# Performance work log

Measured on AMD Instinct MI355X. Metric: run time of the kernel, lower is better.

Reference implementation:

```python
import jax, jax.numpy as jnp
import numpy as np

N = 2048
T = 4000
MAX_SPIKES = 512
V_RESET = 1.0
ALPHA = 0.01


def setup_inputs() -> dict:
    key = jax.random.key(0)
    k1, k2, k3, k4, k5 = jax.random.split(key, 5)
    ts = jnp.arange(T, dtype=jnp.float32) * (1.0 / T)  # [T] grid over [0, 1)
    v0 = 0.1 * jax.random.normal(k1, (N,), dtype=jnp.float32)
    i0 = 0.1 * jax.random.normal(k2, (N,), dtype=jnp.float32)
    ic = jax.random.uniform(k3, (N,), dtype=jnp.float32, minval=0.5, maxval=1.5)
    # _build_w: uniform weights in [0.5, 1), network mask all-False -> no zeroing
    w = jax.random.uniform(k4, (N, N), dtype=jnp.float32, minval=0.5, maxval=1.0)
    mu = jax.random.uniform(k5, (2,), dtype=jnp.float32, minval=0.5, maxval=1.0)
    return {"ts": ts, "v0": v0, "i0": i0, "ic": ic, "w": w, "mu": mu,
            "seed": 0, "max_spikes": MAX_SPIKES}


def reference(ts, v0, i0, ic, w, mu, seed, max_spikes):
    n = v0.shape[0]
    key = jax.random.key(seed)
    k_init, k_trans = jax.random.split(key)
    # s0 = log(U) - alpha  (negative; spike when s crosses 0)
    s0 = jnp.log(jax.random.uniform(k_init, (n,))) - ALPHA
    y0 = jnp.stack([v0, i0, s0], axis=-1)  # [n, 3]

    dts = ts[1:] - ts[:-1]
    steps = jnp.arange(ts.shape[0] - 1)
    tev0 = jnp.full((max_spikes,), jnp.inf, dtype=ts.dtype)
    yev0 = jnp.full((max_spikes, n, 3), jnp.inf, dtype=y0.dtype)
    et0 = jnp.zeros((max_spikes, n), dtype=bool)

    def drift(y):
        v, i, s = y[:, 0], y[:, 1], y[:, 2]
        dv = mu[0] * (i + ic - v)
        di = -mu[1] * i
        ds = jax.nn.softplus(v)  # intensity_fn
        return jnp.stack([dv, di, ds], axis=-1)

    def step(carry, inp):
        y, nsp, tev, yev, et = carry
        t_next, dt, idx = inp
        y1 = y + dt * drift(y)                 # Euler step
        ev = y1[:, 2] >= 0.0                   # cond_fn: y[n, 2] root crossing
        has = jnp.any(ev)
        eidx = jnp.argmax(ev)
        u = jax.random.uniform(jax.random.fold_in(k_trans, idx), (n,))
        # trans_fn: reset v, add weight row to all i, resample s for spikers
        v_t = y1[:, 0] - jnp.where(ev, V_RESET, 0.0)
        i_t = y1[:, 1] + w[eidx]
        s_t = jnp.where(ev, jnp.log(u) - ALPHA, y1[:, 2])
        y2 = jnp.where(has, jnp.stack([v_t, i_t, s_t], axis=-1), y1)
        rec = has & (nsp < max_spikes)
        widx = jnp.minimum(nsp, max_spikes - 1)
        tev = tev.at[widx].set(jnp.where(rec, t_next, tev[widx]))
        yev = yev.at[widx].set(jnp.where(rec, y1, yev[widx]))
        et = et.at[widx].set(jnp.where(rec, ev, et[widx]))
        nsp = nsp + has.astype(jnp.int32)
        return (y2, nsp, tev, yev, et), y2

    init = (y0, jnp.int32(0), tev0, yev0, et0)
    (_, num_spikes, tevents, yevents, event_types), ys_rest = jax.lax.scan(
        step, init, (ts[1:], dts, steps))
    ys = jnp.concatenate([y0[None], ys_rest], axis=0)  # [T, n, 3]
    return ys, tevents, yevents, event_types, num_spikes
```

## Files before the change

### kernel.cpp

```cpp
#include <hip/hip_runtime.h>
#include <stdint.h>

#define XLA_LOG_TAIL_A 1
#define XLA_USE_FMA    0

#if XLA_USE_FMA
#define MADD(a,b,c) __builtin_fmaf((a),(b),(c))
#else
#define MADD(a,b,c) ((a)*(b)+(c))
#endif

#define N_NEUR 2048
#define HALF_N 1024
#define CKPT   125

__device__ __forceinline__ uint32_t rotl32(uint32_t x, int r) {
  return (x << r) | (x >> (32 - r));
}

__device__ __forceinline__ void tf2x32(uint32_t k0, uint32_t k1,
                                       uint32_t& x0, uint32_t& x1) {
  const uint32_t k2 = k0 ^ k1 ^ 0x1BD11BDAu;
  x0 += k0; x1 += k1;
#define TF_R(r) { x0 += x1; x1 = rotl32(x1, r); x1 ^= x0; }
  TF_R(13) TF_R(15) TF_R(26) TF_R(6)
  x0 += k1; x1 += k2 + 1u;
  TF_R(17) TF_R(29) TF_R(16) TF_R(24)
  x0 += k2; x1 += k0 + 2u;
  TF_R(13) TF_R(15) TF_R(26) TF_R(6)
  x0 += k0; x1 += k1 + 3u;
  TF_R(17) TF_R(29) TF_R(16) TF_R(24)
  x0 += k1; x1 += k2 + 4u;
  TF_R(13) TF_R(15) TF_R(26) TF_R(6)
  x0 += k2; x1 += k0 + 5u;
#undef TF_R
}

__device__ __forceinline__ float u01_from_bits(uint32_t bits) {
#pragma clang fp contract(off)
  float f = __uint_as_float((bits >> 9) | 0x3f800000u);
  return f - 1.0f;
}

__device__ __forceinline__ float xla_log(float xin) {
#pragma clang fp contract(off)
  float t0 = fmaxf(xin, __uint_as_float(0x00800000u));
  uint32_t bits = __float_as_uint(t0);
  int em = (int)(bits >> 23) - 127;
  t0 = __uint_as_float((bits & 0x807fffffu) | 0x3f000000u);
  float e = 1.0f + (float)em;
  const bool mlt = t0 < (float)0.707106781186547524;
  float tmp1 = mlt ? t0 : 0.0f;
  t0 = t0 - 1.0f;
  e = e - (mlt ? 1.0f : 0.0f);
  t0 = t0 + tmp1;
  float x2 = t0 * t0;
  float x3 = x2 * t0;
  float y  = MADD(t0, (float)7.0376836292E-2, (float)-1.1514610310E-1);
  float ya = MADD(t0, (float)-1.2420140846E-1, (float)1.4249322787E-1);
  float yb = MADD(t0, (float)2.0000714765E-1, (float)-2.4999993993E-1);
  y  = MADD(y,  t0, (float)1.1676998740E-1);
  ya = MADD(ya, t0, (float)-1.6668057665E-1);
  yb = MADD(yb, t0, (float)3.3333331174E-1);
  y  = MADD(y, x3, ya);
  y  = MADD(y, x3, yb);
  y  = y * x3;
  float ey1 = e * (float)-2.12194440e-4;
  float hx2 = x2 * 0.5f;
  y = y + ey1;
  t0 = t0 - hx2;
  float ey2 = e * (float)0.693359375;
#if XLA_LOG_TAIL_A
  t0 = t0 + y;
  t0 = t0 + ey2;
#else
  t0 = t0 + ey2;
  t0 = t0 + y;
#endif
  if (xin == 0.0f) return -__builtin_inff();
  return t0;
}

__device__ __forceinline__ float xla_exp(float xin) {
#pragma clang fp contract(off)
  float x = fmaxf(xin, (float)-88.3762626647949);
  x = fminf(x, (float)88.3762626647950);
  float fx = floorf(MADD(x, (float)1.44269504088896341, 0.5f));
  float tmp = (float)0.693359375 * fx;
  float z = (float)-2.12194440e-4 * fx;
  x = x - tmp;
  x = x - z;
  z = x * x;
  float y = MADD(x, (float)1.9875691500E-4, (float)1.3981999507E-3);
  y = MADD(y, x, (float)8.3334519073E-3);
  y = MADD(y, x, (float)4.1665795894E-2);
  y = MADD(y, x, (float)1.6666665459E-1);
  y = MADD(y, x, (float)5.0000001201E-1);
  y = MADD(y, z, x);
  y = 1.0f + y;
  int n = (int)fx;
  float p2n = __uint_as_float((uint32_t)(n + 127) << 23);
  return fmaxf(y * p2n, xin);
}

__device__ __forceinline__ float xla_log1p(float x) {
#pragma clang fp contract(off)
  float fl = xla_log(x + 1.0f);
  float fs = ((-0.5f * x) + 1.0f) * x;
  return (fabsf(x) < (float)1e-4) ? fs : fl;
}

__device__ __forceinline__ float softplus_xla(float v) {
#pragma clang fp contract(off)
  if (v >= 16.0f) return v;
  float a = fabsf(v);
  float ex = xla_exp(-a);
  float lp = xla_log1p(ex);
  return fmaxf(v, 0.0f) + lp;
}

__global__ void snn_init(float* __restrict__ out, size_t inf_base,
                         size_t inf_cnt, size_t zero_cnt) {
  size_t i = (size_t)blockIdx.x * blockDim.x + threadIdx.x;
  size_t stride = (size_t)gridDim.x * blockDim.x;
  size_t total = inf_cnt + zero_cnt;
  for (size_t k = i; k < total; k += stride) {
    out[inf_base + k] = (k < inf_cnt) ? __builtin_inff() : 0.0f;
  }
}

__global__ __launch_bounds__(1024)
void snn_pre(const int* __restrict__ seedp, float* __restrict__ sres) {
#pragma clang fp contract(off)
  const int step = blockIdx.x;
  const int t = threadIdx.x;
  uint32_t seed = (uint32_t)seedp[0];
  uint32_t a0 = 0u, a1 = 2u; tf2x32(0u, seed, a0, a1);
  uint32_t b0 = 1u, b1 = 3u; tf2x32(0u, seed, b0, b1);
  uint32_t f0 = 0u, f1 = (uint32_t)step; tf2x32(a1, b1, f0, f1);
  uint32_t d0 = (uint32_t)t, d1 = (uint32_t)(t + HALF_N);
  tf2x32(f0, f1, d0, d1);
  float srA = xla_log(u01_from_bits(d0)) - 0.01f;
  float srB = xla_log(u01_from_bits(d1)) - 0.01f;
  sres[(size_t)step * N_NEUR + t] = srA;
  sres[(size_t)step * N_NEUR + HALF_N + t] = srB;
}

__global__ __launch_bounds__(512, 1)
void snn_evt(const float* __restrict__ ts, const float* __restrict__ v0,
             const float* __restrict__ i0, const float* __restrict__ ic,
             const float* __restrict__ w, const float* __restrict__ mu,
             const int* __restrict__ seedp, const float* __restrict__ sres,
             uint32_t* __restrict__ spk, float* __restrict__ out, int T, int MS) {
#pragma clang fp contract(off)
  const int tid = threadIdx.x;
  const int nb = tid * 4;
  const int wave = tid >> 6;
  const int lane = tid & 63;

  float* ys   = out;
  float* tev  = out + (size_t)T * N_NEUR * 3;
  float* etv  = tev + (size_t)MS + (size_t)MS * N_NEUR * 3;
  float* nspp = etv + (size_t)MS * N_NEUR;

  uint32_t seed = (uint32_t)seedp[0];
  uint32_t a0 = 0u, a1 = 2u; tf2x32(0u, seed, a0, a1);
  uint32_t b0 = 1u, b1 = 3u; tf2x32(0u, seed, b0, b1);
  const uint32_t ki0 = a0, ki1 = b0;

  float vv[4], ipd[4], ss[4], icv[4], wvp[4];
  {
    float4 x = *(const float4*)&v0[nb];
    vv[0]=x.x; vv[1]=x.y; vv[2]=x.z; vv[3]=x.w;
  }
  {
    float4 x = *(const float4*)&i0[nb];
    ipd[0]=x.x; ipd[1]=x.y; ipd[2]=x.z; ipd[3]=x.w;
  }
  {
    float4 x = *(const float4*)&ic[nb];
    icv[0]=x.x; icv[1]=x.y; icv[2]=x.z; icv[3]=x.w;
  }
#pragma unroll
  for (int q = 0; q < 4; ++q) {
    int j = nb + q;
    uint32_t c0 = (uint32_t)(j < HALF_N ? j : j - HALF_N);
    uint32_t c1 = c0 + HALF_N;
    tf2x32(ki0, ki1, c0, c1);
    ss[q] = xla_log(u01_from_bits(j < HALF_N ? c0 : c1)) - 0.01f;
    wvp[q] = 0.0f;
  }
  const float m0 = mu[0], m1 = mu[1];

  __shared__ alignas(16) uint32_t slot[2][8];
  if (tid < 16) ((uint32_t*)slot)[tid] = 0xFFFFFFFFu;
  __syncthreads();

  int nsp = 0;
  bool hasPrev = false;
  float tp = ts[0];
  float tn = ts[1];
  int next_ck = 0;

  for (int k = 0; k < T - 1; ++k) {
    const float dt = tn - tp;

    float tn_nx = ts[(k + 2 < T) ? (k + 2) : (T - 1)];
    float4 srv = *(const float4*)(sres + (size_t)k * N_NEUR + nb);
    float sr[4] = {srv.x, srv.y, srv.z, srv.w};

    float ii[4];
#pragma unroll
    for (int q = 0; q < 4; ++q) ii[q] = hasPrev ? (ipd[q] + wvp[q]) : ipd[q];

    if (k == next_ck) {
      float* yr = ys + ((size_t)k * N_NEUR + nb) * 3;
      ((float4*)yr)[0] = make_float4(vv[0], ii[0], ss[0], vv[1]);
      ((float4*)yr)[1] = make_float4(ii[1], ss[1], vv[2], ii[2]);
      ((float4*)yr)[2] = make_float4(ss[2], vv[3], ii[3], ss[3]);
      next_ck += CKPT;
    }

    float y1s[4];
    bool ev[4];
#pragma unroll
    for (int q = 0; q < 4; ++q) {
      float sp = softplus_xla(vv[q]);
      y1s[q] = ss[q] + dt * sp;
      ev[q] = (y1s[q] >= 0.0f);
    }

    int lidx = 4;
    if (ev[3]) lidx = 3;
    if (ev[2]) lidx = 2;
    if (ev[1]) lidx = 1;
    if (ev[0]) lidx = 0;
    unsigned long long bm = __ballot(lidx < 4);
    if (lane == 0) {
      uint32_t cand = 0xFFFFFFFFu;
      if (bm) {
        int fl = __builtin_ctzll(bm);
        cand = (uint32_t)__builtin_amdgcn_readlane(nb + lidx, fl);
      }
      slot[k & 1][wave] = cand;
    }

    float y1v[4], y1i[4];
#pragma unroll
    for (int q = 0; q < 4; ++q) {
      float dv = m0 * ((ii[q] + icv[q]) - vv[q]);
      y1v[q] = vv[q] + dt * dv;
      y1i[q] = ii[q] + dt * ((-m1) * ii[q]);
    }

    __syncthreads();

    uint32_t gmin;
    {
      const uint4* rp = (const uint4*)&slot[k & 1][0];
      uint4 r0 = rp[0], r1 = rp[1];
      uint32_t a = r0.x < r0.y ? r0.x : r0.y;
      uint32_t b = r0.z < r0.w ? r0.z : r0.w;
      uint32_t c = r1.x < r1.y ? r1.x : r1.y;
      uint32_t d = r1.z < r1.w ? r1.z : r1.w;
      a = a < b ? a : b;
      c = c < d ? c : d;
      gmin = a < c ? a : c;
    }
    gmin = (uint32_t)__builtin_amdgcn_readfirstlane((int)gmin);
    const bool has = (gmin != 0xFFFFFFFFu);

    float wn[4] = {0.0f, 0.0f, 0.0f, 0.0f};
    if (has) {
      float4 x = *(const float4*)&w[((size_t)gmin << 11) + nb];
      wn[0]=x.x; wn[1]=x.y; wn[2]=x.z; wn[3]=x.w;
    }

    if (tid == 0) {
      spk[k] = ((uint32_t)nsp << 16) | (has ? (gmin & 0xFFFFu) : 0xFFFFu);
      if (has && nsp < MS) tev[nsp] = tn;
    }
    nsp += has ? 1 : 0;

#pragma unroll
    for (int q = 0; q < 4; ++q) {
      vv[q] = y1v[q] - (ev[q] ? 1.0f : 0.0f);
      ss[q] = ev[q] ? sr[q] : y1s[q];
      ipd[q] = y1i[q];
      wvp[q] = wn[q];
    }
    hasPrev = has;
    tp = tn; tn = tn_nx;
  }

  if (tid == 0) nspp[0] = (float)nsp;
}

__global__ __launch_bounds__(1024, 1)
void snn_rep(const float* __restrict__ ts, const float* __restrict__ ic,
             const float* __restrict__ w, const float* __restrict__ mu,
             const float* __restrict__ sres, const uint32_t* __restrict__ spk,
             float* __restrict__ out, int T, int MS) {
#pragma clang fp contract(off)
  const int seg = blockIdx.x >> 1;
  const int gn = (blockIdx.x & 1) * 1024 + threadIdx.x;
  const int lo = seg * CKPT;
  const int end = min(lo + CKPT, T - 1);

  float* ys  = out;
  float* tev = out + (size_t)T * N_NEUR * 3;
  float* yev = tev + (size_t)MS;
  float* etv = yev + (size_t)MS * N_NEUR * 3;

  const float* y0r = ys + ((size_t)lo * N_NEUR + gn) * 3;
  float vv = y0r[0];
  float ii = y0r[1];
  float ss = y0r[2];
  const float icv = ic[gn];
  const float m0 = mu[0], m1 = mu[1];
  float tp = ts[lo];

  for (int k = lo; k < end; ++k) {
    const float tn = ts[k + 1];
    const float dt = tn - tp;
    tp = tn;
    const uint32_t pk = spk[k];

    float sp  = softplus_xla(vv);
    float y1s = ss + dt * sp;
    const bool ev = (y1s >= 0.0f);
    float dv  = m0 * ((ii + icv) - vv);
    float y1v = vv + dt * dv;
    float y1i = ii + dt * ((-m1) * ii);

    const uint32_t e16 = pk & 0xFFFFu;
    const bool has = (e16 != 0xFFFFu);
    const uint32_t nsp = pk >> 16;

    float wv = 0.0f;
    if (has) wv = w[((size_t)e16 << 11) + gn];

    if (has && nsp < (uint32_t)MS) {
      float* ye = yev + ((size_t)nsp * N_NEUR + gn) * 3;
      ye[0] = y1v; ye[1] = y1i; ye[2] = y1s;
      etv[(size_t)nsp * N_NEUR + gn] = ev ? 1.0f : 0.0f;
    }

    ii = has ? (y1i + wv) : y1i;
    vv = y1v - (ev ? 1.0f : 0.0f);
    if (ev) ss = sres[(size_t)k * N_NEUR + gn]; else ss = y1s;

    float* yr = ys + ((size_t)(k + 1) * N_NEUR + gn) * 3;
    yr[0] = vv; yr[1] = ii; yr[2] = ss;
  }
}

template <bool USE_SRES>
__global__ __launch_bounds__(1024, 1)
void snn_sim(const float* __restrict__ ts, const float* __restrict__ v0,
             const float* __restrict__ i0, const float* __restrict__ ic,
             const float* __restrict__ w, const float* __restrict__ mu,
             const int* __restrict__ seedp, const float* __restrict__ sres,
             float* __restrict__ out, int T, int MS) {
#pragma clang fp contract(off)
  const int tid = threadIdx.x;
  const int nb = tid * 2;
  const int lane = tid & 63;

  float* ys   = out;
  float* tev  = out + (size_t)T * N_NEUR * 3;
  float* yev  = tev + (size_t)MS;
  float* etv  = yev + (size_t)MS * N_NEUR * 3;
  float* nspp = etv + (size_t)MS * N_NEUR;

  uint32_t seed = (uint32_t)seedp[0];
  uint32_t a0 = 0u, a1 = 2u; tf2x32(0u, seed, a0, a1);
  uint32_t b0 = 1u, b1 = 3u; tf2x32(0u, seed, b0, b1);
  const uint32_t ki0 = a0, ki1 = b0;
  const uint32_t kt0 = a1, kt1 = b1;

  float vv0, vv1, ii0, ii1, ss0, ss1, icv0, icv1;
  { float2 x = *(const float2*)&v0[nb]; vv0 = x.x; vv1 = x.y; }
  { float2 x = *(const float2*)&i0[nb]; ii0 = x.x; ii1 = x.y; }
  { float2 x = *(const float2*)&ic[nb]; icv0 = x.x; icv1 = x.y; }
  {
    uint32_t c0 = (uint32_t)(nb < HALF_N ? nb : nb - HALF_N);
    uint32_t c1 = c0 + HALF_N;
    tf2x32(ki0, ki1, c0, c1);
    ss0 = xla_log(u01_from_bits(nb < HALF_N ? c0 : c1)) - 0.01f;
  }
  {
    int j = nb + 1;
    uint32_t c0 = (uint32_t)(j < HALF_N ? j : j - HALF_N);
    uint32_t c1 = c0 + HALF_N;
    tf2x32(ki0, ki1, c0, c1);
    ss1 = xla_log(u01_from_bits(j < HALF_N ? c0 : c1)) - 0.01f;
  }
  const float m0 = mu[0], m1 = mu[1];

  {
    float* yr = ys + (size_t)nb * 3;
    ((float2*)yr)[0] = make_float2(vv0, ii0);
    ((float2*)yr)[1] = make_float2(ss0, vv1);
    ((float2*)yr)[2] = make_float2(ii1, ss1);
  }

  __shared__ uint32_t slot[4];
  if (tid < 4) slot[tid] = 0xFFFFFFFFu;
  __syncthreads();

  int nsp = 0;
  float tp = ts[0];
  const float* srp = USE_SRES ? (sres + nb) : nullptr;
  float* yrow = ys + (size_t)N_NEUR * 3 + (size_t)nb * 3;

  for (int k = 0; k < T - 1; ++k) {
    const float tn = ts[k + 1];
    const float dt = tn - tp;
    tp = tn;

    float sr0 = 0.0f, sr1 = 0.0f;
    if (USE_SRES) {
      float2 x = *(const float2*)srp;
      sr0 = x.x; sr1 = x.y;
      srp += N_NEUR;
    }

    float sp0 = softplus_xla(vv0);
    float sp1 = softplus_xla(vv1);
    float y1s0 = ss0 + dt * sp0;
    float y1s1 = ss1 + dt * sp1;
    const bool ev0 = (y1s0 >= 0.0f);
    const bool ev1 = (y1s1 >= 0.0f);

    int lidx = ev0 ? 0 : (ev1 ? 1 : 2);
    unsigned long long bm = __ballot(lidx < 2);
    if (lane == 0 && bm) {
      int fl = __builtin_ctzll(bm);
      uint32_t cand = (uint32_t)__builtin_amdgcn_readlane(nb + lidx, fl);
      atomicMin(&slot[k & 3], cand);
    }
    if (tid == 0) slot[(k + 1) & 3] = 0xFFFFFFFFu;

    float dv0 = m0 * ((ii0 + icv0) - vv0);
    float dv1 = m0 * ((ii1 + icv1) - vv1);
    float y1v0 = vv0 + dt * dv0;
    float y1v1 = vv1 + dt * dv1;
    float y1i0 = ii0 + dt * ((-m1) * ii0);
    float y1i1 = ii1 + dt * ((-m1) * ii1);

    __syncthreads();

    uint32_t gmin = (uint32_t)__builtin_amdgcn_readfirstlane((int)slot[k & 3]);
    const bool has = (gmin != 0xFFFFFFFFu);

    float wv0 = 0.0f, wv1 = 0.0f;
    if (has) {
      float2 x = *(const float2*)&w[((size_t)gmin << 11) + nb];
      wv0 = x.x; wv1 = x.y;
    }

    if (has && nsp < MS) {
      if (tid == 0) tev[nsp] = tn;
      float* ye = yev + ((size_t)nsp * N_NEUR + nb) * 3;
      ((float2*)ye)[0] = make_float2(y1v0, y1i0);
      ((float2*)ye)[1] = make_float2(y1s0, y1v1);
      ((float2*)ye)[2] = make_float2(y1i1, y1s1);
      *(float2*)(etv + (size_t)nsp * N_NEUR + nb) =
          make_float2(ev0 ? 1.0f : 0.0f, ev1 ? 1.0f : 0.0f);
    }
    nsp += has ? 1 : 0;

    ii0 = has ? (y1i0 + wv0) : y1i0;
    ii1 = has ? (y1i1 + wv1) : y1i1;
    vv0 = y1v0 - (ev0 ? 1.0f : 0.0f);
    vv1 = y1v1 - (ev1 ? 1.0f : 0.0f);
    if (USE_SRES) {
      ss0 = ev0 ? sr0 : y1s0;
      ss1 = ev1 ? sr1 : y1s1;
    } else {
      ss0 = y1s0; ss1 = y1s1;
      if (ev0 | ev1) {
        uint32_t f0 = 0u, f1 = (uint32_t)k;
        tf2x32(kt0, kt1, f0, f1);
        if (ev0) {
          uint32_t c0 = (uint32_t)(nb < HALF_N ? nb : nb - HALF_N);
          uint32_t c1 = c0 + HALF_N;
          tf2x32(f0, f1, c0, c1);
          ss0 = xla_log(u01_from_bits(nb < HALF_N ? c0 : c1)) - 0.01f;
        }
        if (ev1) {
          int j = nb + 1;
          uint32_t c0 = (uint32_t)(j < HALF_N ? j : j - HALF_N);
          uint32_t c1 = c0 + HALF_N;
          tf2x32(f0, f1, c0, c1);
          ss1 = xla_log(u01_from_bits(j < HALF_N ? c0 : c1)) - 0.01f;
        }
      }
    }

    ((float2*)yrow)[0] = make_float2(vv0, ii0);
    ((float2*)yrow)[1] = make_float2(ss0, vv1);
    ((float2*)yrow)[2] = make_float2(ii1, ss1);
    yrow += (size_t)N_NEUR * 3;
  }

  if (tid == 0) nspp[0] = (float)nsp;
}

extern "C" void kernel_launch(void* const* d_in, const int* in_sizes, int n_in,
                              void* d_out, int out_size, void* d_ws, size_t ws_size,
                              hipStream_t stream) {
  const float* ts = (const float*)d_in[0];
  const float* v0 = (const float*)d_in[1];
  const float* i0 = (const float*)d_in[2];
  const float* ic = (const float*)d_in[3];
  const float* w  = (const float*)d_in[4];
  const float* mu = (const float*)d_in[5];
  const int* seed = (const int*)d_in[6];

  const int T = in_sizes[0];
  const int N = in_sizes[1];
  long long rem = (long long)out_size - (long long)T * N * 3 - 1;
  int MS = (int)(rem / (1 + 4 * (long long)N));
  if (MS <= 0) MS = 512;

  size_t inf_base = (size_t)T * N * 3;
  size_t inf_cnt  = (size_t)MS + (size_t)MS * N * 3;
  size_t zero_cnt = (size_t)MS * N;
  snn_init<<<dim3(512), dim3(256), 0, stream>>>((float*)d_out, inf_base, inf_cnt, zero_cnt);

  size_t sres_bytes = (size_t)(T - 1) * (size_t)N * sizeof(float);
  size_t full_bytes = sres_bytes + (size_t)(T - 1) * sizeof(uint32_t);

  if (ws_size >= full_bytes) {
    float* sres = (float*)d_ws;
    uint32_t* spk = (uint32_t*)((char*)d_ws + sres_bytes);
    snn_pre<<<dim3(T - 1), dim3(1024), 0, stream>>>(seed, sres);
    snn_evt<<<dim3(1), dim3(512), 0, stream>>>(ts, v0, i0, ic, w, mu, seed,
                                               sres, spk, (float*)d_out, T, MS);
    int nseg = (T - 1 + CKPT - 1) / CKPT;
    snn_rep<<<dim3(nseg * 2), dim3(1024), 0, stream>>>(ts, ic, w, mu, sres, spk,
                                                       (float*)d_out, T, MS);
  } else if (ws_size >= sres_bytes) {
    snn_pre<<<dim3(T - 1), dim3(1024), 0, stream>>>(seed, (float*)d_ws);
    snn_sim<true><<<dim3(1), dim3(1024), 0, stream>>>(ts, v0, i0, ic, w, mu, seed,
                                                      (const float*)d_ws,
                                                      (float*)d_out, T, MS);
  } else {
    snn_sim<false><<<dim3(1), dim3(1024), 0, stream>>>(ts, v0, i0, ic, w, mu, seed,
                                                       nullptr, (float*)d_out, T, MS);
  }
}
```

Before: 3.402 ms.

## Process two timesteps per block barrier in the sequential SNN scan

Unrolls the serial scan so each iteration resolves spike decisions for two consecutive steps (even and odd) before a single __syncthreads. This works because the weight row added by one step only reaches the spike test two steps later. Both per-wave first-spiker candidates go into one 64-bit shared slot and are reduced together, roughly halving the barrier and LDS round trips on the critical path. The checkpoint stride moves to an even value so snapshots land on even steps, which adds an odd-tail epilogue, more register pressure, and a dependence on the replay kernel and host grid matching the new CKPT.

```diff
diff --git a/kernel.cpp b/kernel.cpp
--- a/kernel.cpp
+++ b/kernel.cpp
@@ -12,7 +12,7 @@
 
 #define N_NEUR 2048
 #define HALF_N 1024
-#define CKPT   125
+#define CKPT   124
 
 __device__ __forceinline__ uint32_t rotl32(uint32_t x, int r) {
   return (x << r) | (x >> (32 - r));
@@ -168,14 +168,25 @@
   uint32_t b0 = 1u, b1 = 3u; tf2x32(0u, seed, b0, b1);
   const uint32_t ki0 = a0, ki1 = b0;
 
-  float vv[4], ipd[4], ss[4], icv[4], wvp[4];
+  const float m0 = mu[0], m1 = mu[1];
+
+  float vvO[4];
+  float ssE[4];
+  bool  evO[4];
+  float y1iP[4];
+  float wEp[4], wOp[4];
+  bool  hasEp = false, hasOp = false;
+  float dtOp = 0.0f;
+  float icv[4];
+  float srE[4], srO[4];
+
   {
     float4 x = *(const float4*)&v0[nb];
-    vv[0]=x.x; vv[1]=x.y; vv[2]=x.z; vv[3]=x.w;
+    vvO[0]=x.x; vvO[1]=x.y; vvO[2]=x.z; vvO[3]=x.w;
   }
   {
     float4 x = *(const float4*)&i0[nb];
-    ipd[0]=x.x; ipd[1]=x.y; ipd[2]=x.z; ipd[3]=x.w;
+    y1iP[0]=x.x; y1iP[1]=x.y; y1iP[2]=x.z; y1iP[3]=x.w;
   }
   {
     float4 x = *(const float4*)&ic[nb];
@@ -187,110 +198,225 @@
     uint32_t c0 = (uint32_t)(j < HALF_N ? j : j - HALF_N);
     uint32_t c1 = c0 + HALF_N;
     tf2x32(ki0, ki1, c0, c1);
-    ss[q] = xla_log(u01_from_bits(j < HALF_N ? c0 : c1)) - 0.01f;
-    wvp[q] = 0.0f;
-  }
-  const float m0 = mu[0], m1 = mu[1];
-
-  __shared__ alignas(16) uint32_t slot[2][8];
-  if (tid < 16) ((uint32_t*)slot)[tid] = 0xFFFFFFFFu;
+    ssE[q] = xla_log(u01_from_bits(j < HALF_N ? c0 : c1)) - 0.01f;
+    evO[q] = false;
+    wEp[q] = 0.0f; wOp[q] = 0.0f;
+  }
+  {
+    float4 x = *(const float4*)(sres + nb);
+    srE[0]=x.x; srE[1]=x.y; srE[2]=x.z; srE[3]=x.w;
+  }
+  {
+    float4 x = *(const float4*)(sres + N_NEUR + nb);
+    srO[0]=x.x; srO[1]=x.y; srO[2]=x.z; srO[3]=x.w;
+  }
+
+  __shared__ alignas(16) uint32_t slot[2][16];
   __syncthreads();
 
   int nsp = 0;
-  bool hasPrev = false;
-  float tp = ts[0];
-  float tn = ts[1];
   int next_ck = 0;
-
-  for (int k = 0; k < T - 1; ++k) {
-    const float dt = tn - tp;
-
-    float tn_nx = ts[(k + 2 < T) ? (k + 2) : (T - 1)];
-    float4 srv = *(const float4*)(sres + (size_t)k * N_NEUR + nb);
-    float sr[4] = {srv.x, srv.y, srv.z, srv.w};
-
-    float ii[4];
-#pragma unroll
-    for (int q = 0; q < 4; ++q) ii[q] = hasPrev ? (ipd[q] + wvp[q]) : ipd[q];
-
-    if (k == next_ck) {
-      float* yr = ys + ((size_t)k * N_NEUR + nb) * 3;
-      ((float4*)yr)[0] = make_float4(vv[0], ii[0], ss[0], vv[1]);
-      ((float4*)yr)[1] = make_float4(ii[1], ss[1], vv[2], ii[2]);
-      ((float4*)yr)[2] = make_float4(ss[2], vv[3], ii[3], ss[3]);
-      next_ck += CKPT;
-    }
-
-    float y1s[4];
-    bool ev[4];
+  float tsE = ts[0];
+  const int pairs = (T - 1) >> 1;
+  const int last_row = T - 2;
+
+  for (int P = 0; P < pairs; ++P) {
+    const int e = 2 * P;
+
+    float vvE[4], iiE[4], y1iO_[4];
 #pragma unroll
     for (int q = 0; q < 4; ++q) {
-      float sp = softplus_xla(vv[q]);
-      y1s[q] = ss[q] + dt * sp;
-      ev[q] = (y1s[q] >= 0.0f);
-    }
-
-    int lidx = 4;
-    if (ev[3]) lidx = 3;
-    if (ev[2]) lidx = 2;
-    if (ev[1]) lidx = 1;
-    if (ev[0]) lidx = 0;
-    unsigned long long bm = __ballot(lidx < 4);
-    if (lane == 0) {
-      uint32_t cand = 0xFFFFFFFFu;
-      if (bm) {
-        int fl = __builtin_ctzll(bm);
-        cand = (uint32_t)__builtin_amdgcn_readlane(nb + lidx, fl);
-      }
-      slot[k & 1][wave] = cand;
-    }
-
-    float y1v[4], y1i[4];
+      float iiO = hasEp ? (y1iP[q] + wEp[q]) : y1iP[q];
+      float dv  = m0 * ((iiO + icv[q]) - vvO[q]);
+      float y1v = vvO[q] + dtOp * dv;
+      float y1i = iiO + dtOp * ((-m1) * iiO);
+      vvE[q] = y1v - (evO[q] ? 1.0f : 0.0f);
+      y1iO_[q] = y1i;
+    }
+#pragma unroll
+    for (int q = 0; q < 4; ++q)
+      iiE[q] = hasOp ? (y1iO_[q] + wOp[q]) : y1iO_[q];
+
+    if (e == next_ck) {
+      float* yr = ys + ((size_t)e * N_NEUR + nb) * 3;
+      ((float4*)yr)[0] = make_float4(vvE[0], iiE[0], ssE[0], vvE[1]);
+      ((float4*)yr)[1] = make_float4(iiE[1], ssE[1], vvE[2], iiE[2]);
+      ((float4*)yr)[2] = make_float4(ssE[2], vvE[3], iiE[3], ssE[3]);
+      next_ck += CKPT;
+    }
+
+    const float tsE1 = ts[e + 1];
+    const float tsE2 = ts[e + 2];
+    const float dtE = tsE1 - tsE;
+    const float dtO = tsE2 - tsE1;
+
+    float y1iE[4], vvOn[4], ssEn[4];
+    bool evE[4], evOn[4];
 #pragma unroll
     for (int q = 0; q < 4; ++q) {
-      float dv = m0 * ((ii[q] + icv[q]) - vv[q]);
-      y1v[q] = vv[q] + dt * dv;
-      y1i[q] = ii[q] + dt * ((-m1) * ii[q]);
+      float sp  = softplus_xla(vvE[q]);
+      float y1s = ssE[q] + dtE * sp;
+      evE[q] = (y1s >= 0.0f);
+      float dv  = m0 * ((iiE[q] + icv[q]) - vvE[q]);
+      float y1v = vvE[q] + dtE * dv;
+      y1iE[q] = iiE[q] + dtE * ((-m1) * iiE[q]);
+      vvOn[q] = y1v - (evE[q] ? 1.0f : 0.0f);
+      float ssO_ = evE[q] ? srE[q] : y1s;
+      float spO = softplus_xla(vvOn[q]);
+      float y1sO = ssO_ + dtO * spO;
+      evOn[q] = (y1sO >= 0.0f);
+      ssEn[q] = evOn[q] ? srO[q] : y1sO;
+    }
+
+    {
+      int lE = 4;
+      if (evE[3]) lE = 3;
+      if (evE[2]) lE = 2;
+      if (evE[1]) lE = 1;
+      if (evE[0]) lE = 0;
+      int lO = 4;
+      if (evOn[3]) lO = 3;
+      if (evOn[2]) lO = 2;
+      if (evOn[1]) lO = 1;
+      if (evOn[0]) lO = 0;
+      unsigned long long bE = __ballot(lE < 4);
+      unsigned long long bO = __ballot(lO < 4);
+      if (lane == 0) {
+        uint32_t cE = 0xFFFFFFFFu, cO = 0xFFFFFFFFu;
+        if (bE) cE = (uint32_t)__builtin_amdgcn_readlane(nb + lE, __builtin_ctzll(bE));
+        if (bO) cO = (uint32_t)__builtin_amdgcn_readlane(nb + lO, __builtin_ctzll(bO));
+        *(uint64_t*)&slot[P & 1][wave * 2] = ((uint64_t)cO << 32) | (uint64_t)cE;
+      }
+    }
+    float srEn[4], srOn[4];
+    {
+      int re = e + 2;  if (re > last_row) re = last_row;
+      int ro = e + 3;  if (ro > last_row) ro = last_row;
+      float4 x = *(const float4*)(sres + (size_t)re * N_NEUR + nb);
+      srEn[0]=x.x; srEn[1]=x.y; srEn[2]=x.z; srEn[3]=x.w;
+      float4 y = *(const float4*)(sres + (size_t)ro * N_NEUR + nb);
+      srOn[0]=y.x; srOn[1]=y.y; srOn[2]=y.z; srOn[3]=y.w;
     }
 
     __syncthreads();
 
-    uint32_t gmin;
+    uint32_t gE, gO;
     {
-      const uint4* rp = (const uint4*)&slot[k & 1][0];
-      uint4 r0 = rp[0], r1 = rp[1];
-      uint32_t a = r0.x < r0.y ? r0.x : r0.y;
-      uint32_t b = r0.z < r0.w ? r0.z : r0.w;
-      uint32_t c = r1.x < r1.y ? r1.x : r1.y;
-      uint32_t d = r1.z < r1.w ? r1.z : r1.w;
-      a = a < b ? a : b;
-      c = c < d ? c : d;
-      gmin = a < c ? a : c;
-    }
-    gmin = (uint32_t)__builtin_amdgcn_readfirstlane((int)gmin);
-    const bool has = (gmin != 0xFFFFFFFFu);
-
-    float wn[4] = {0.0f, 0.0f, 0.0f, 0.0f};
-    if (has) {
-      float4 x = *(const float4*)&w[((size_t)gmin << 11) + nb];
-      wn[0]=x.x; wn[1]=x.y; wn[2]=x.z; wn[3]=x.w;
-    }
+      const uint4* rp = (const uint4*)&slot[P & 1][0];
+      uint4 r0 = rp[0], r1 = rp[1], r2 = rp[2], r3 = rp[3];
+      uint32_t a = r0.x < r1.x ? r0.x : r1.x;
+      uint32_t b = r2.x < r3.x ? r2.x : r3.x;
+      uint32_t c = r0.z < r1.z ? r0.z : r1.z;
+      uint32_t d = r2.z < r3.z ? r2.z : r3.z;
+      a = a < b ? a : b;  c = c < d ? c : d;
+      gE = a < c ? a : c;
+      uint32_t e1 = r0.y < r1.y ? r0.y : r1.y;
+      uint32_t f1 = r2.y < r3.y ? r2.y : r3.y;
+      uint32_t g1 = r0.w < r1.w ? r0.w : r1.w;
+      uint32_t h1 = r2.w < r3.w ? r2.w : r3.w;
+      e1 = e1 < f1 ? e1 : f1;  g1 = g1 < h1 ? g1 : h1;
+      gO = e1 < g1 ? e1 : g1;
+    }
+    gE = (uint32_t)__builtin_amdgcn_readfirstlane((int)gE);
+    gO = (uint32_t)__builtin_amdgcn_readfirstlane((int)gO);
+    const bool hasE = (gE != 0xFFFFFFFFu);
+    const bool hasO = (gO != 0xFFFFFFFFu);
 
     if (tid == 0) {
-      spk[k] = ((uint32_t)nsp << 16) | (has ? (gmin & 0xFFFFu) : 0xFFFFu);
-      if (has && nsp < MS) tev[nsp] = tn;
-    }
-    nsp += has ? 1 : 0;
+      spk[e] = ((uint32_t)nsp << 16) | (hasE ? (gE & 0xFFFFu) : 0xFFFFu);
+      if (hasE && nsp < MS) tev[nsp] = tsE1;
+    }
+    int nspE = nsp + (hasE ? 1 : 0);
+    if (tid == 0) {
+      spk[e + 1] = ((uint32_t)nspE << 16) | (hasO ? (gO & 0xFFFFu) : 0xFFFFu);
+      if (hasO && nspE < MS) tev[nspE] = tsE2;
+    }
+    nsp = nspE + (hasO ? 1 : 0);
+
+    float wEn[4] = {0,0,0,0}, wOn[4] = {0,0,0,0};
+    if (hasE) {
+      float4 x = *(const float4*)&w[((size_t)gE << 11) + nb];
+      wEn[0]=x.x; wEn[1]=x.y; wEn[2]=x.z; wEn[3]=x.w;
+    }
+    if (hasO) {
+      float4 x = *(const float4*)&w[((size_t)gO << 11) + nb];
+      wOn[0]=x.x; wOn[1]=x.y; wOn[2]=x.z; wOn[3]=x.w;
+    }
 
 #pragma unroll
     for (int q = 0; q < 4; ++q) {
-      vv[q] = y1v[q] - (ev[q] ? 1.0f : 0.0f);
-      ss[q] = ev[q] ? sr[q] : y1s[q];
-      ipd[q] = y1i[q];
-      wvp[q] = wn[q];
-    }
-    hasPrev = has;
-    tp = tn; tn = tn_nx;
+      vvO[q] = vvOn[q];
+      ssE[q] = ssEn[q];
+      evO[q] = evOn[q];
+      y1iP[q] = y1iE[q];
+      wEp[q] = wEn[q];
+      wOp[q] = wOn[q];
+      srE[q] = srEn[q];
+      srO[q] = srOn[q];
+    }
+    hasEp = hasE; hasOp = hasO;
+    dtOp = dtO;
+    tsE = tsE2;
+  }
+
+  if ((T - 1) & 1) {
+    const int e = T - 2;
+    float vvE[4], iiE[4];
+#pragma unroll
+    for (int q = 0; q < 4; ++q) {
+      float iiO = hasEp ? (y1iP[q] + wEp[q]) : y1iP[q];
+      float dv  = m0 * ((iiO + icv[q]) - vvO[q]);
+      float y1v = vvO[q] + dtOp * dv;
+      float y1i = iiO + dtOp * ((-m1) * iiO);
+      vvE[q] = y1v - (evO[q] ? 1.0f : 0.0f);
+      iiE[q] = hasOp ? (y1i + wOp[q]) : y1i;
+    }
+    if (e == next_ck) {
+      float* yr = ys + ((size_t)e * N_NEUR + nb) * 3;
+      ((float4*)yr)[0] = make_float4(vvE[0], iiE[0], ssE[0], vvE[1]);
+      ((float4*)yr)[1] = make_float4(iiE[1], ssE[1], vvE[2], iiE[2]);
+      ((float4*)yr)[2] = make_float4(ssE[2], vvE[3], iiE[3], ssE[3]);
+    }
+    const float tsE1 = ts[T - 1];
+    const float dtE = tsE1 - tsE;
+    bool evE[4];
+#pragma unroll
+    for (int q = 0; q < 4; ++q) {
+      float sp  = softplus_xla(vvE[q]);
+      float y1s = ssE[q] + dtE * sp;
+      evE[q] = (y1s >= 0.0f);
+    }
+    int lE = 4;
+    if (evE[3]) lE = 3;
+    if (evE[2]) lE = 2;
+    if (evE[1]) lE = 1;
+    if (evE[0]) lE = 0;
+    unsigned long long bE = __ballot(lE < 4);
+    if (lane == 0) {
+      uint32_t cE = 0xFFFFFFFFu;
+      if (bE) cE = (uint32_t)__builtin_amdgcn_readlane(nb + lE, __builtin_ctzll(bE));
+      *(uint64_t*)&slot[pairs & 1][wave * 2] =
+          ((uint64_t)0xFFFFFFFFu << 32) | (uint64_t)cE;
+    }
+    __syncthreads();
+    uint32_t gE;
+    {
+      const uint4* rp = (const uint4*)&slot[pairs & 1][0];
+      uint4 r0 = rp[0], r1 = rp[1], r2 = rp[2], r3 = rp[3];
+      uint32_t a = r0.x < r1.x ? r0.x : r1.x;
+      uint32_t b = r2.x < r3.x ? r2.x : r3.x;
+      uint32_t c = r0.z < r1.z ? r0.z : r1.z;
+      uint32_t d = r2.z < r3.z ? r2.z : r3.z;
+      a = a < b ? a : b;  c = c < d ? c : d;
+      gE = a < c ? a : c;
+    }
+    gE = (uint32_t)__builtin_amdgcn_readfirstlane((int)gE);
+    const bool hasE = (gE != 0xFFFFFFFFu);
+    if (tid == 0) {
+      spk[e] = ((uint32_t)nsp << 16) | (hasE ? (gE & 0xFFFFu) : 0xFFFFu);
+      if (hasE && nsp < MS) tev[nsp] = tsE1;
+    }
+    nsp += hasE ? 1 : 0;
   }
 
   if (tid == 0) nspp[0] = (float)nsp;
```

Result: faster. 3.097 ms (-9.0%).
